# Kernel tuning notes

Measured on AMD Instinct MI355X. Metric: run time of the kernel, lower is better.

Reference implementation:

```python
import jax, jax.numpy as jnp
import numpy as np

MAX_DELAY = 64   # kernel taps (module default 100; 64 = 4*block_size)
DT = 1.0
K_MIN = 0.1      # floor on storage constant for numerical safety


def _causal_depthwise_conv(x, k):
    """x: [B, C, T], k: [C, Tk].  y[b,c,t] = sum_tau k[c,tau] * x[b,c,t-tau]."""
    Tk = k.shape[1]
    return jax.lax.conv_general_dilated(
        x, k[:, None, ::-1], window_strides=(1,),
        padding=[(Tk - 1, 0)],
        feature_group_count=k.shape[0],
        dimension_numbers=('NCH', 'OIH', 'NCH'))


def _linear_storage_irf(params):
    """Per-node linear-reservoir impulse response, discretized to MAX_DELAY taps.
    params: [N, 2]; uses col 0 as (unconstrained) storage constant. -> [N, Tk]."""
    kst = jax.nn.softplus(params[:, 0]) + K_MIN              # [N]
    t = jnp.arange(MAX_DELAY, dtype=params.dtype) * DT       # [Tk]
    h = jnp.exp(-t[None, :] / kst[:, None]) * (DT / kst[:, None])
    return h / jnp.sum(h, axis=1, keepdims=True)             # unit mass


def setup_inputs() -> dict:
    key = jax.random.key(0)
    k1, k2, k3, k4 = jax.random.split(key, 4)
    B, N, T, E = 2, 4096, 2048, 8192
    x = jax.random.normal(k1, (B, N, T), dtype=jnp.float32)
    params = jax.random.normal(k2, (N, 2), dtype=jnp.float32)
    edge_src = jax.random.randint(k3, (E,), 0, N)
    edge_tgt = jax.random.randint(k4, (E,), 0, N)
    return {"x": x, "params": params, "edge_src": edge_src, "edge_tgt": edge_tgt}


def reference(x, params, edge_src, edge_tgt):
    B, N, T = x.shape
    # --- RoutingIRFAggregator: per-pair routing kernels ---
    h = _linear_storage_irf(params)                 # [N, Tk]
    h_src = h[edge_src]                             # [E, Tk] irregular gather
    h_tgt = h[edge_tgt]                             # [E, Tk]
    # edge kernel = causal composition (convolution) of src and tgt IRFs, truncated to Tk
    K_edge = _causal_depthwise_conv(h_src[None], h_tgt)[0]   # [E, Tk]
    # include diagonal (self) pairs since runoff_to_output=False
    K = jnp.concatenate([K_edge, h], axis=0)                 # [P, Tk], P = E + N
    src_all = jnp.concatenate([edge_src, jnp.arange(N)])
    tgt_all = jnp.concatenate([edge_tgt, jnp.arange(N)])
    # --- BlockSparseCausalConv: per-pair causal conv then scatter-add to targets ---
    xg = x[:, src_all, :]                           # [B, P, T] irregular gather
    yp = _causal_depthwise_conv(xg, K)              # [B, P, T]
    y = jax.ops.segment_sum(yp.transpose(1, 0, 2), tgt_all, num_segments=N)  # [N, B, T]
    return y.transpose(1, 0, 2)                     # [B, N, T]
```

## Files before the change

### kernel.cpp

```cpp
#include <hip/hip_runtime.h>
#include <math.h>

static constexpr int NN = 4096;
static constexpr int TT = 2048;
static constexpr int EE = 8192;
static constexpr int TK = 64;
static constexpr int CAP = 32;
static constexpr int HALO = 80;
static constexpr int XROW = HALO + TT;
static constexpr int TABS = 104;

typedef __attribute__((ext_vector_type(8))) short        short8v;
typedef __attribute__((ext_vector_type(4))) float        float4v;
typedef __attribute__((ext_vector_type(2))) unsigned int uint2v;

__device__ __forceinline__ unsigned cvtpk_bf16(float lo, float hi) {
    unsigned r;
    asm("v_cvt_pk_bf16_f32 %0, %1, %2" : "=v"(r) : "v"(lo), "v"(hi));
    return r;
}

__global__ void prep_kernel(const float* __restrict__ params,
                            const float* __restrict__ x,
                            float* __restrict__ hirf, unsigned short* __restrict__ hb,
                            unsigned short* __restrict__ xb, int* __restrict__ cnt) {
    int blk = blockIdx.x;
    if (blk < 1024) {
        #pragma unroll
        for (int rr = 0; rr < 8; ++rr) {
            size_t row = (size_t)blk * 8 + rr;
            const float4* src = reinterpret_cast<const float4*>(x) + row * (TT / 4);
            unsigned short* drow = xb + row * XROW;
            if (threadIdx.x < 10)
                reinterpret_cast<uint4*>(drow)[threadIdx.x] = make_uint4(0, 0, 0, 0);
            #pragma unroll
            for (int c = 0; c < 2; ++c) {
                int u = threadIdx.x + 256 * c;
                float4 v = src[u];
                uint2v o; o.x = cvtpk_bf16(v.x, v.y); o.y = cvtpk_bf16(v.z, v.w);
                *reinterpret_cast<uint2v*>(drow + HALO + 4 * u) = o;
            }
        }
    } else if (blk < 2048) {
        int t = (blk - 1024) * 256 + threadIdx.x;
        int node = t >> 6, lane = t & 63;
        float p = params[node * 2];
        float sp = fmaxf(p, 0.f) + log1pf(expf(-fabsf(p)));
        float kst = sp + 0.1f;
        float inv = 1.0f / kst;
        float hv = expf(-(float)lane * inv) * inv;
        float s = hv;
        #pragma unroll
        for (int d = 1; d < 64; d <<= 1) s += __shfl_xor(s, d, 64);
        float val = hv / s;
        hirf[node * TK + lane] = val;
        hb[node * TK + lane] = (unsigned short)(cvtpk_bf16(val, val) & 0xffffu);
    } else {
        int i = (blk - 2048) * 256 + threadIdx.x;
        if (i < NN) cnt[i] = 0;
    }
}

__global__ void kedge_kernel(const float* __restrict__ hirf,
                             const int* __restrict__ esrc, const int* __restrict__ etgt,
                             unsigned short* __restrict__ Kb, int* __restrict__ cnt,
                             int2* __restrict__ elist2) {
    __shared__ float s_src[4][TK];
    __shared__ float s_tgt[4][TK];
    int lane = threadIdx.x & 63;
    int grp  = threadIdx.x >> 6;
    int e = blockIdx.x * 4 + grp;
    int s = esrc[e], t = etgt[e];
    s_src[grp][lane] = hirf[s * TK + lane];
    s_tgt[grp][lane] = hirf[t * TK + lane];
    __syncthreads();
    float acc = 0.f;
    for (int tau = 0; tau <= lane; ++tau)
        acc += s_tgt[grp][tau] * s_src[grp][lane - tau];
    Kb[e * TK + lane] = (unsigned short)(cvtpk_bf16(acc, acc) & 0xffffu);
    if (lane == 0) {
        int pos = atomicAdd(&cnt[t], 1);
        if (pos < CAP) elist2[t * CAP + pos] = make_int2(e, s);
    }
}

__global__ __launch_bounds__(256)
void conv_dg_kernel(const unsigned short* __restrict__ xb,
                    const unsigned short* __restrict__ hb,
                    const unsigned short* __restrict__ Kb,
                    const int2* __restrict__ elist2,
                    const int* __restrict__ cnt,
                    float* __restrict__ y) {
    __shared__ unsigned short tab[4][16 * TABS];

    const int tid    = threadIdx.x;
    const int wv     = tid >> 6;
    const int l      = tid & 63;
    const int lane16 = l & 15;
    const int h      = l >> 4;
    const int hlo    = h & 1, hhi = h >> 1;
    const int b      = wv >> 1;
    const int half   = wv & 1;
    const int tgt    = blockIdx.x;
    unsigned short* mytab = tab[wv];

    {
        int z = l & 15;
        #pragma unroll
        for (int k = 0; k < 4; ++k) {
            int r = (l >> 4) + 4 * k;
            mytab[TABS * r + z] = 0;
            mytab[TABS * r + ((z <= r) ? z + 16 : 80 + z)] = 0;
        }
    }

    float4v acc[4];
    #pragma unroll
    for (int T = 0; T < 4; ++T) acc[T] = (float4v){0.f, 0.f, 0.f, 0.f};

    int deg = __builtin_amdgcn_readfirstlane(cnt[tgt]);
    if (deg > CAP) deg = CAP;
    const int nr = deg + 1;

    int srcCur = tgt;
    unsigned short kvCur = hb[(size_t)tgt * TK + l];
    int eN = 0, sN = 0;
    if (nr > 1) {
        int2 m = elist2[tgt * CAP];
        eN = __builtin_amdgcn_readfirstlane(m.x);
        sN = __builtin_amdgcn_readfirstlane(m.y);
    }

    for (int i = 0; i < nr; ++i) {
        const unsigned short* xr = xb + ((size_t)b * NN + srcCur) * XROW;

        short8v Bv[4][3];
        #pragma unroll
        for (int T = 0; T < 4; ++T) {
            const int bb = HALO + 16 * (64 * half + 16 * T + lane16) + 8 * hlo;
            #pragma unroll
            for (int c = 0; c < 3; ++c)
                Bv[T][c] = *reinterpret_cast<const short8v*>(&xr[bb - 16 * (2 * c + hhi)]);
        }

        #pragma unroll
        for (int r = 0; r < 16; ++r)
            mytab[TABS * r + 80 + r - l] = kvCur;

        const int abase = TABS * lane16 + 80 + 8 * hlo;
        short8v A0 = *reinterpret_cast<const short8v*>(&mytab[abase - 16 * (0 + hhi)]);
        short8v A1 = *reinterpret_cast<const short8v*>(&mytab[abase - 16 * (2 + hhi)]);
        short8v A2 = *reinterpret_cast<const short8v*>(&mytab[abase - 16 * (4 + hhi)]);

        int srcNext = srcCur;
        unsigned short kvNext = kvCur;
        if (i + 1 < nr) {
            srcNext = sN;
            kvNext  = Kb[(size_t)eN * TK + l];
            if (i + 2 < nr) {
                int2 m = elist2[tgt * CAP + i + 1];
                eN = __builtin_amdgcn_readfirstlane(m.x);
                sN = __builtin_amdgcn_readfirstlane(m.y);
            }
        }

        #pragma unroll
        for (int T = 0; T < 4; ++T) {
            acc[T] = __builtin_amdgcn_mfma_f32_16x16x32_bf16(A0, Bv[T][0], acc[T], 0, 0, 0);
            acc[T] = __builtin_amdgcn_mfma_f32_16x16x32_bf16(A1, Bv[T][1], acc[T], 0, 0, 0);
            acc[T] = __builtin_amdgcn_mfma_f32_16x16x32_bf16(A2, Bv[T][2], acc[T], 0, 0, 0);
        }

        srcCur = srcNext;
        kvCur  = kvNext;
    }

    float* yrow = y + ((size_t)b * NN + tgt) * TT;
    #pragma unroll
    for (int T = 0; T < 4; ++T) {
        int tb = 16 * (64 * half + 16 * T + lane16) + 4 * h;
        float4v v = acc[T];
        __builtin_nontemporal_store(v, reinterpret_cast<float4v*>(yrow + tb));
    }
}

extern "C" void kernel_launch(void* const* d_in, const int* in_sizes, int n_in,
                              void* d_out, int out_size, void* d_ws, size_t ws_size,
                              hipStream_t stream) {
    const float* x      = (const float*)d_in[0];
    const float* params = (const float*)d_in[1];
    const int*   esrc   = (const int*)d_in[2];
    const int*   etgt   = (const int*)d_in[3];
    float* y = (float*)d_out;

    char* w = (char*)d_ws;
    float*          hirf   = (float*)w;          w += (size_t)NN * TK * 4;
    unsigned short* hb     = (unsigned short*)w; w += (size_t)NN * TK * 2;
    unsigned short* Kb     = (unsigned short*)w; w += (size_t)EE * TK * 2;
    int*            cnt    = (int*)w;            w += (size_t)NN * 4;
    int2*           elist2 = (int2*)w;           w += (size_t)NN * CAP * 8;
    unsigned short* xb     = (unsigned short*)w; w += (size_t)2 * NN * XROW * 2;
    (void)ws_size;

    hipLaunchKernelGGL(prep_kernel, dim3(2064), dim3(256), 0, stream,
                       params, x, hirf, hb, xb, cnt);
    hipLaunchKernelGGL(kedge_kernel, dim3(EE / 4), dim3(256), 0, stream,
                       hirf, esrc, etgt, Kb, cnt, elist2);
    hipLaunchKernelGGL(conv_dg_kernel, dim3(NN), dim3(256), 0, stream,
                       xb, hb, Kb, elist2, cnt, y);
}
```

Baseline: 56.24 us.

## Factor edge kernels into two-pass conv: per-node IRF then gather-sum and target conv

Replaces the per-edge composed kernels with a two-pass scheme. Pass A convolves every node's input with its own IRF and stores the result as bf16 z. Pass B sums x_tgt with z of all incoming sources, then convolves that sum once with the target IRF. This removes the per-edge kernel composition and the per-edge MFMA convolutions, and the bf16 x staging is replaced by in-block conversion into shared memory. The factoring drops the truncation of the composed kernel to 64 taps, adding tail terms up to 127 lags, and adds a bf16 rounding of the intermediate z, so results may drift from the reference.

```diff
diff --git a/kernel.cpp b/kernel.cpp
--- a/kernel.cpp
+++ b/kernel.cpp
@@ -7,42 +7,73 @@
 static constexpr int TK = 64;
 static constexpr int CAP = 32;
 static constexpr int HALO = 80;
-static constexpr int XROW = HALO + TT;
-static constexpr int TABS = 104;
+static constexpr int TABS = 96;
 
 typedef __attribute__((ext_vector_type(8))) short        short8v;
 typedef __attribute__((ext_vector_type(4))) float        float4v;
-typedef __attribute__((ext_vector_type(2))) unsigned int uint2v;
 
 __device__ __forceinline__ unsigned cvtpk_bf16(float lo, float hi) {
     unsigned r;
     asm("v_cvt_pk_bf16_f32 %0, %1, %2" : "=v"(r) : "v"(lo), "v"(hi));
     return r;
 }
+__device__ __forceinline__ float bf2f(unsigned short u) {
+    union { unsigned u; float f; } v; v.u = ((unsigned)u) << 16; return v.f;
+}
+
+struct __align__(16) ConvLds {
+    unsigned short xrow[HALO + TT];
+    unsigned short tab[16 * TABS];
+};
+
+#define TAB_ZERO_INIT(lds)                                            \
+    {                                                                 \
+        int z_ = tid & 15;                                            \
+        _Pragma("unroll")                                             \
+        for (int rr_ = 0; rr_ < 2; ++rr_) {                           \
+            int r2_ = (tid >> 4) + 8 * rr_;                           \
+            (lds).tab[TABS * r2_ + z_] = 0;                           \
+            (lds).tab[TABS * r2_ + ((z_ <= r2_) ? z_ + 16 : 80 + z_)] = 0; \
+        }                                                             \
+    }
+
+#define TAB_VALUE(lds, kb)                                            \
+    {                                                                 \
+        int rg_ = tid >> 6;                                           \
+        _Pragma("unroll")                                             \
+        for (int rr_ = 0; rr_ < 8; ++rr_) {                           \
+            int r_ = rg_ * 8 + rr_;                                   \
+            (lds).tab[TABS * r_ + 80 + r_ - l] = (kb);                \
+        }                                                             \
+    }
+
+#define CONV_COMPUTE(lds, acc)                                        \
+    {                                                                 \
+        const unsigned short* tab_ = (lds).tab;                       \
+        const unsigned short* xv_  = (lds).xrow;                      \
+        const int abase_ = TABS * lane16 + 80 + 8 * hlo;              \
+        short8v A0 = *reinterpret_cast<const short8v*>(&tab_[abase_ - 16 * (0 + hhi)]); \
+        short8v A1 = *reinterpret_cast<const short8v*>(&tab_[abase_ - 16 * (2 + hhi)]); \
+        short8v A2 = *reinterpret_cast<const short8v*>(&tab_[abase_ - 16 * (4 + hhi)]); \
+        _Pragma("unroll")                                             \
+        for (int T = 0; T < 4; ++T) {                                 \
+            const int bb_ = HALO + 16 * (64 * half + 16 * T + lane16) + 8 * hlo; \
+            short8v B0 = *reinterpret_cast<const short8v*>(&xv_[bb_ - 16 * (0 + hhi)]); \
+            acc[T] = __builtin_amdgcn_mfma_f32_16x16x32_bf16(A0, B0, acc[T], 0, 0, 0); \
+            short8v B1 = *reinterpret_cast<const short8v*>(&xv_[bb_ - 16 * (2 + hhi)]); \
+            acc[T] = __builtin_amdgcn_mfma_f32_16x16x32_bf16(A1, B1, acc[T], 0, 0, 0); \
+            short8v B2 = *reinterpret_cast<const short8v*>(&xv_[bb_ - 16 * (4 + hhi)]); \
+            acc[T] = __builtin_amdgcn_mfma_f32_16x16x32_bf16(A2, B2, acc[T], 0, 0, 0); \
+        }                                                             \
+    }
 
 __global__ void prep_kernel(const float* __restrict__ params,
-                            const float* __restrict__ x,
-                            float* __restrict__ hirf, unsigned short* __restrict__ hb,
-                            unsigned short* __restrict__ xb, int* __restrict__ cnt) {
+                            const int* __restrict__ esrc, const int* __restrict__ etgt,
+                            unsigned short* __restrict__ hb,
+                            int* __restrict__ cnt, int* __restrict__ slist) {
     int blk = blockIdx.x;
     if (blk < 1024) {
-        #pragma unroll
-        for (int rr = 0; rr < 8; ++rr) {
-            size_t row = (size_t)blk * 8 + rr;
-            const float4* src = reinterpret_cast<const float4*>(x) + row * (TT / 4);
-            unsigned short* drow = xb + row * XROW;
-            if (threadIdx.x < 10)
-                reinterpret_cast<uint4*>(drow)[threadIdx.x] = make_uint4(0, 0, 0, 0);
-            #pragma unroll
-            for (int c = 0; c < 2; ++c) {
-                int u = threadIdx.x + 256 * c;
-                float4 v = src[u];
-                uint2v o; o.x = cvtpk_bf16(v.x, v.y); o.y = cvtpk_bf16(v.z, v.w);
-                *reinterpret_cast<uint2v*>(drow + HALO + 4 * u) = o;
-            }
-        }
-    } else if (blk < 2048) {
-        int t = (blk - 1024) * 256 + threadIdx.x;
+        int t = blk * 256 + threadIdx.x;
         int node = t >> 6, lane = t & 63;
         float p = params[node * 2];
         float sp = fmaxf(p, 0.f) + log1pf(expf(-fabsf(p)));
@@ -53,127 +84,128 @@
         #pragma unroll
         for (int d = 1; d < 64; d <<= 1) s += __shfl_xor(s, d, 64);
         float val = hv / s;
-        hirf[node * TK + lane] = val;
         hb[node * TK + lane] = (unsigned short)(cvtpk_bf16(val, val) & 0xffffu);
     } else {
-        int i = (blk - 2048) * 256 + threadIdx.x;
-        if (i < NN) cnt[i] = 0;
-    }
-}
-
-__global__ void kedge_kernel(const float* __restrict__ hirf,
-                             const int* __restrict__ esrc, const int* __restrict__ etgt,
-                             unsigned short* __restrict__ Kb, int* __restrict__ cnt,
-                             int2* __restrict__ elist2) {
-    __shared__ float s_src[4][TK];
-    __shared__ float s_tgt[4][TK];
-    int lane = threadIdx.x & 63;
-    int grp  = threadIdx.x >> 6;
-    int e = blockIdx.x * 4 + grp;
-    int s = esrc[e], t = etgt[e];
-    s_src[grp][lane] = hirf[s * TK + lane];
-    s_tgt[grp][lane] = hirf[t * TK + lane];
-    __syncthreads();
-    float acc = 0.f;
-    for (int tau = 0; tau <= lane; ++tau)
-        acc += s_tgt[grp][tau] * s_src[grp][lane - tau];
-    Kb[e * TK + lane] = (unsigned short)(cvtpk_bf16(acc, acc) & 0xffffu);
-    if (lane == 0) {
+        int e = (blk - 1024) * 256 + threadIdx.x;
+        int t = etgt[e], s = esrc[e];
         int pos = atomicAdd(&cnt[t], 1);
-        if (pos < CAP) elist2[t * CAP + pos] = make_int2(e, s);
-    }
-}
-
-__global__ __launch_bounds__(256)
-void conv_dg_kernel(const unsigned short* __restrict__ xb,
-                    const unsigned short* __restrict__ hb,
-                    const unsigned short* __restrict__ Kb,
-                    const int2* __restrict__ elist2,
-                    const int* __restrict__ cnt,
-                    float* __restrict__ y) {
-    __shared__ unsigned short tab[4][16 * TABS];
-
+        if (pos < CAP) slist[t * CAP + pos] = s;
+    }
+}
+
+__global__ __launch_bounds__(128)
+void passA_kernel(const float* __restrict__ x,
+                  const unsigned short* __restrict__ hb,
+                  unsigned short* __restrict__ z) {
+    __shared__ ConvLds lds;
     const int tid    = threadIdx.x;
-    const int wv     = tid >> 6;
+    const int bid    = blockIdx.x;
+    const int b      = bid & 1;
+    const int node   = bid >> 1;
     const int l      = tid & 63;
     const int lane16 = l & 15;
     const int h      = l >> 4;
     const int hlo    = h & 1, hhi = h >> 1;
-    const int b      = wv >> 1;
-    const int half   = wv & 1;
-    const int tgt    = blockIdx.x;
-    unsigned short* mytab = tab[wv];
-
-    {
-        int z = l & 15;
-        #pragma unroll
-        for (int k = 0; k < 4; ++k) {
-            int r = (l >> 4) + 4 * k;
-            mytab[TABS * r + z] = 0;
-            mytab[TABS * r + ((z <= r) ? z + 16 : 80 + z)] = 0;
-        }
-    }
+    const int half   = tid >> 6;
+
+    const float4* xr = reinterpret_cast<const float4*>(x + ((size_t)b * NN + node) * TT);
+    float4 px[4];
+    #pragma unroll
+    for (int c = 0; c < 4; ++c) px[c] = xr[tid + 128 * c];
+    unsigned short kb = hb[(size_t)node * TK + l];
+
+    for (int idx = tid; idx < HALO; idx += 128) lds.xrow[idx] = 0;
+    TAB_ZERO_INIT(lds);
+
+    #pragma unroll
+    for (int c = 0; c < 4; ++c) {
+        int u = tid + 128 * c;
+        unsigned lo = cvtpk_bf16(px[c].x, px[c].y);
+        unsigned hi = cvtpk_bf16(px[c].z, px[c].w);
+        *reinterpret_cast<uint2*>(&lds.xrow[HALO + 4 * u]) = make_uint2(lo, hi);
+    }
+    TAB_VALUE(lds, kb);
+    __syncthreads();
 
     float4v acc[4];
     #pragma unroll
     for (int T = 0; T < 4; ++T) acc[T] = (float4v){0.f, 0.f, 0.f, 0.f};
-
+    CONV_COMPUTE(lds, acc);
+
+    unsigned short* zr = z + ((size_t)b * NN + node) * TT;
+    #pragma unroll
+    for (int T = 0; T < 4; ++T) {
+        int tb = 16 * (64 * half + 16 * T + lane16) + 4 * h;
+        uint2 o = make_uint2(cvtpk_bf16(acc[T][0], acc[T][1]),
+                             cvtpk_bf16(acc[T][2], acc[T][3]));
+        *reinterpret_cast<uint2*>(&zr[tb]) = o;
+    }
+}
+
+__global__ __launch_bounds__(128)
+void passB_kernel(const float* __restrict__ x,
+                  const unsigned short* __restrict__ z,
+                  const unsigned short* __restrict__ hb,
+                  const int* __restrict__ slist,
+                  const int* __restrict__ cnt,
+                  float* __restrict__ y) {
+    __shared__ ConvLds lds;
+    const int tid    = threadIdx.x;
+    const int bid    = blockIdx.x;
+    const int b      = bid & 1;
+    const int tgt    = bid >> 1;
+    const int l      = tid & 63;
+    const int lane16 = l & 15;
+    const int h      = l >> 4;
+    const int hlo    = h & 1, hhi = h >> 1;
+    const int half   = tid >> 6;
+
+    const float4* xr = reinterpret_cast<const float4*>(x + ((size_t)b * NN + tgt) * TT);
+    float4 xa = xr[2 * tid], xb4 = xr[2 * tid + 1];
+    float4 xc = xr[2 * tid + 256], xd = xr[2 * tid + 257];
+    unsigned short kb = hb[(size_t)tgt * TK + l];
     int deg = __builtin_amdgcn_readfirstlane(cnt[tgt]);
     if (deg > CAP) deg = CAP;
-    const int nr = deg + 1;
-
-    int srcCur = tgt;
-    unsigned short kvCur = hb[(size_t)tgt * TK + l];
-    int eN = 0, sN = 0;
-    if (nr > 1) {
-        int2 m = elist2[tgt * CAP];
-        eN = __builtin_amdgcn_readfirstlane(m.x);
-        sN = __builtin_amdgcn_readfirstlane(m.y);
-    }
-
-    for (int i = 0; i < nr; ++i) {
-        const unsigned short* xr = xb + ((size_t)b * NN + srcCur) * XROW;
-
-        short8v Bv[4][3];
+    int sCur = 0;
+    if (deg > 0) sCur = __builtin_amdgcn_readfirstlane(slist[tgt * CAP]);
+
+    for (int idx = tid; idx < HALO; idx += 128) lds.xrow[idx] = 0;
+    TAB_ZERO_INIT(lds);
+
+    float w[16];
+    w[0] = xa.x;  w[1] = xa.y;  w[2] = xa.z;  w[3] = xa.w;
+    w[4] = xb4.x; w[5] = xb4.y; w[6] = xb4.z; w[7] = xb4.w;
+    w[8] = xc.x;  w[9] = xc.y;  w[10] = xc.z; w[11] = xc.w;
+    w[12] = xd.x; w[13] = xd.y; w[14] = xd.z; w[15] = xd.w;
+
+    for (int j = 0; j < deg; ++j) {
+        const short8v* zr = reinterpret_cast<const short8v*>(z + ((size_t)b * NN + sCur) * TT);
+        short8v z0 = zr[tid];
+        short8v z1 = zr[tid + 128];
+        if (j + 1 < deg) sCur = __builtin_amdgcn_readfirstlane(slist[tgt * CAP + j + 1]);
         #pragma unroll
-        for (int T = 0; T < 4; ++T) {
-            const int bb = HALO + 16 * (64 * half + 16 * T + lane16) + 8 * hlo;
-            #pragma unroll
-            for (int c = 0; c < 3; ++c)
-                Bv[T][c] = *reinterpret_cast<const short8v*>(&xr[bb - 16 * (2 * c + hhi)]);
+        for (int k = 0; k < 8; ++k) {
+            w[k]     += bf2f((unsigned short)z0[k]);
+            w[8 + k] += bf2f((unsigned short)z1[k]);
         }
-
-        #pragma unroll
-        for (int r = 0; r < 16; ++r)
-            mytab[TABS * r + 80 + r - l] = kvCur;
-
-        const int abase = TABS * lane16 + 80 + 8 * hlo;
-        short8v A0 = *reinterpret_cast<const short8v*>(&mytab[abase - 16 * (0 + hhi)]);
-        short8v A1 = *reinterpret_cast<const short8v*>(&mytab[abase - 16 * (2 + hhi)]);
-        short8v A2 = *reinterpret_cast<const short8v*>(&mytab[abase - 16 * (4 + hhi)]);
-
-        int srcNext = srcCur;
-        unsigned short kvNext = kvCur;
-        if (i + 1 < nr) {
-            srcNext = sN;
-            kvNext  = Kb[(size_t)eN * TK + l];
-            if (i + 2 < nr) {
-                int2 m = elist2[tgt * CAP + i + 1];
-                eN = __builtin_amdgcn_readfirstlane(m.x);
-                sN = __builtin_amdgcn_readfirstlane(m.y);
-            }
-        }
-
-        #pragma unroll
-        for (int T = 0; T < 4; ++T) {
-            acc[T] = __builtin_amdgcn_mfma_f32_16x16x32_bf16(A0, Bv[T][0], acc[T], 0, 0, 0);
-            acc[T] = __builtin_amdgcn_mfma_f32_16x16x32_bf16(A1, Bv[T][1], acc[T], 0, 0, 0);
-            acc[T] = __builtin_amdgcn_mfma_f32_16x16x32_bf16(A2, Bv[T][2], acc[T], 0, 0, 0);
-        }
-
-        srcCur = srcNext;
-        kvCur  = kvNext;
-    }
+    }
+
+    {
+        uint4 o;
+        o.x = cvtpk_bf16(w[0], w[1]); o.y = cvtpk_bf16(w[2], w[3]);
+        o.z = cvtpk_bf16(w[4], w[5]); o.w = cvtpk_bf16(w[6], w[7]);
+        *reinterpret_cast<uint4*>(&lds.xrow[HALO + 8 * tid]) = o;
+        o.x = cvtpk_bf16(w[8], w[9]);   o.y = cvtpk_bf16(w[10], w[11]);
+        o.z = cvtpk_bf16(w[12], w[13]); o.w = cvtpk_bf16(w[14], w[15]);
+        *reinterpret_cast<uint4*>(&lds.xrow[HALO + 1024 + 8 * tid]) = o;
+    }
+    TAB_VALUE(lds, kb);
+    __syncthreads();
+
+    float4v acc[4];
+    #pragma unroll
+    for (int T = 0; T < 4; ++T) acc[T] = (float4v){0.f, 0.f, 0.f, 0.f};
+    CONV_COMPUTE(lds, acc);
 
     float* yrow = y + ((size_t)b * NN + tgt) * TT;
     #pragma unroll
@@ -194,18 +226,16 @@
     float* y = (float*)d_out;
 
     char* w = (char*)d_ws;
-    float*          hirf   = (float*)w;          w += (size_t)NN * TK * 4;
-    unsigned short* hb     = (unsigned short*)w; w += (size_t)NN * TK * 2;
-    unsigned short* Kb     = (unsigned short*)w; w += (size_t)EE * TK * 2;
-    int*            cnt    = (int*)w;            w += (size_t)NN * 4;
-    int2*           elist2 = (int2*)w;           w += (size_t)NN * CAP * 8;
-    unsigned short* xb     = (unsigned short*)w; w += (size_t)2 * NN * XROW * 2;
+    unsigned short* hb    = (unsigned short*)w; w += (size_t)NN * TK * 2;
+    int*            cnt   = (int*)w;            w += (size_t)NN * 4;
+    int*            slist = (int*)w;            w += (size_t)NN * CAP * 4;
+    unsigned short* z     = (unsigned short*)w; w += (size_t)2 * NN * TT * 2;
     (void)ws_size;
 
-    hipLaunchKernelGGL(prep_kernel, dim3(2064), dim3(256), 0, stream,
-                       params, x, hirf, hb, xb, cnt);
-    hipLaunchKernelGGL(kedge_kernel, dim3(EE / 4), dim3(256), 0, stream,
-                       hirf, esrc, etgt, Kb, cnt, elist2);
-    hipLaunchKernelGGL(conv_dg_kernel, dim3(NN), dim3(256), 0, stream,
-                       xb, hb, Kb, elist2, cnt, y);
-}
+    hipMemsetAsync(cnt, 0, (size_t)NN * 4, stream);
+    hipLaunchKernelGGL(prep_kernel, dim3(1056), dim3(256), 0, stream,
+                       params, esrc, etgt, hb, cnt, slist);
+    hipLaunchKernelGGL(passA_kernel, dim3(NN * 2), dim3(128), 0, stream, x, hb, z);
+    hipLaunchKernelGGL(passB_kernel, dim3(NN * 2), dim3(128), 0, stream,
+                       x, z, hb, slist, cnt, y);
+}
```

Result: slower. 57.99 us (+3.1%).
